# Performance work log

Hardware: AMD Instinct MI355X
Metric: run time of the kernel (lower is better)

Reference implementation:

```python
import jax, jax.numpy as jnp
import numpy as np

N, H, E, ATTR = 50000, 256, 800000, 107


def _ln(x, g, b, eps=1e-5):
    mu = jnp.mean(x, axis=-1, keepdims=True)
    v = jnp.mean((x - mu) ** 2, axis=-1, keepdims=True)
    return (x - mu) * jax.lax.rsqrt(v + eps) * g + b


def _gcn(x, src, dst, ew, W, b, n):
    # PyG GCNConv with edge_weight: add self-loops (weight 1), symmetric norm
    loop = jnp.arange(n)
    src = jnp.concatenate([src, loop])
    dst = jnp.concatenate([dst, loop])
    ew = jnp.concatenate([ew, jnp.ones((n,), ew.dtype)])
    deg = jax.ops.segment_sum(ew, dst, num_segments=n)  # [n]
    dinv = jnp.where(deg > 0, jax.lax.rsqrt(deg), 0.0)
    norm = dinv[src] * ew * dinv[dst]  # [E+n]
    h = x @ W.T  # [n,H] linear transform first
    agg = jax.ops.segment_sum(norm[:, None] * h[src], dst, num_segments=n)
    return agg + b


def setup_inputs() -> dict:
    key = jax.random.key(0)
    ks = jax.random.split(key, 12)
    s = 1.0 / np.sqrt(H)
    return {
        "x_struct": jax.random.normal(ks[0], (N, H), jnp.float32),
        "edge_index_bold": jax.random.randint(ks[1], (2, E), 0, N),
        "edge_attr_bold": jax.random.uniform(ks[2], (E,), jnp.float32),  # positive weights
        "edge_index_temp": jax.random.randint(ks[3], (2, E), 0, N),
        "edge_attr_temp": jax.random.uniform(ks[4], (E, ATTR), jnp.float32),
        "Wb": jax.random.normal(ks[5], (H, H), jnp.float32) * s,
        "bb": jnp.zeros((H,), jnp.float32),
        "Wt": jax.random.normal(ks[6], (H, H), jnp.float32) * s,
        "bt": jnp.zeros((H,), jnp.float32),
        "W1": jax.random.normal(ks[7], (H, ATTR), jnp.float32) * (1.0 / np.sqrt(ATTR)),
        "b1": jnp.zeros((H,), jnp.float32),
        "g1": jnp.ones((H,), jnp.float32),
        "be1": jnp.zeros((H,), jnp.float32),
        "W2": jax.random.normal(ks[8], (1, H), jnp.float32) * 0.01,
        "b2": jnp.ones((1,), jnp.float32),  # keep temporal edge weights positive
        "gs": jnp.ones((H,), jnp.float32),
        "bs": jnp.zeros((H,), jnp.float32),
        "gt": jnp.ones((H,), jnp.float32),
        "btn": jnp.zeros((H,), jnp.float32),
    }


def reference(x_struct, edge_attr_bold, edge_attr_temp, Wb, bb, Wt, bt,
              W1, b1, g1, be1, W2, b2, gs, bs, gt, btn,
              edge_index_bold, edge_index_temp):
    x = x_struct
    orig = x
    # BOLD-correlation GCN stage: gcn -> residual -> LN -> ReLU
    out = _gcn(x, edge_index_bold[0], edge_index_bold[1], edge_attr_bold, Wb, bb, N)
    x = jax.nn.relu(_ln(out + x, gs, bs))
    # temporal edge-weight MLP: Linear(107->H) -> LN -> ReLU -> Linear(H->1) -> squeeze
    h = jax.nn.relu(_ln(edge_attr_temp @ W1.T + b1, g1, be1))
    w = (h @ W2.T + b2)[:, 0]  # [E]
    # temporal GCN stage: gcn -> residual -> LN -> ReLU
    out = _gcn(x, edge_index_temp[0], edge_index_temp[1], w, Wt, bt, N)
    x = jax.nn.relu(_ln(out + x, gt, btn))
    # final residual with original input through struct_norm
    return _ln(x + orig, gs, bs)
```

## Files before the change

### kernel.cpp

```cpp
#include <hip/hip_runtime.h>

#define HDIM 256
#define KA 107
#define KAP 128

typedef short bf16x8 __attribute__((ext_vector_type(8)));
typedef float f32x4 __attribute__((ext_vector_type(4)));
typedef unsigned short ushort_t;

__device__ inline unsigned short f2bf(float f) {
    union { float f; unsigned u; } v; v.f = f;
    unsigned r = v.u + 0x7fff + ((v.u >> 16) & 1);
    return (unsigned short)(r >> 16);
}

__device__ inline unsigned cvt_pk_bf16(float a, float b) {
    unsigned r;
    asm("v_cvt_pk_bf16_f32 %0, %1, %2" : "=v"(r) : "v"(a), "v"(b));
    return r;
}

__device__ inline float bf_lo(unsigned u) { union { unsigned v; float f; } x; x.v = u << 16; return x.f; }
__device__ inline float bf_hi(unsigned u) { union { unsigned v; float f; } x; x.v = u & 0xffff0000u; return x.f; }

__device__ inline float4 guarded_load4(const float* p, size_t off, size_t tot) {
    if (off + 4 <= tot) return *(const float4*)(p + off);
    float4 r = {0.f, 0.f, 0.f, 0.f};
    float* rr = (float*)&r;
    for (int e = 0; e < 4; ++e) if (off + e < tot) rr[e] = p[off + e];
    return r;
}


__global__ void init_deg_kernel(float* deg, int n) {
    int i = blockIdx.x * 256 + threadIdx.x;
    if (i < n) deg[i] = 1.0f;
}

__global__ void hist_kernel(const int* __restrict__ dst, const float* __restrict__ w,
                            float* deg, int* cnt, int ne) {
    int e = blockIdx.x * 256 + threadIdx.x;
    if (e < ne) {
        int d = dst[e];
        atomicAdd(&deg[d], w[e]);
        atomicAdd(&cnt[d], 1);
    }
}

__global__ void rsqrt_kernel(float* deg, int n) {
    int i = blockIdx.x * 256 + threadIdx.x;
    if (i < n) { float d = deg[i]; deg[i] = d > 0.f ? rsqrtf(d) : 0.f; }
}

__global__ void f32_to_bf16_kernel(const float* __restrict__ in, ushort_t* __restrict__ out, int n4) {
    int i = blockIdx.x * 256 + threadIdx.x;
    if (i < n4) {
        float4 v = ((const float4*)in)[i];
        uint2 o;
        o.x = cvt_pk_bf16(v.x, v.y);
        o.y = cvt_pk_bf16(v.z, v.w);
        ((uint2*)out)[i] = o;
    }
}

__global__ __launch_bounds__(1024) void scan_kernel(const int* __restrict__ cnt,
                                                    int* __restrict__ rptr,
                                                    int* __restrict__ cur, int n) {
    const int per = (n + 1023) / 1024;
    const int tid = threadIdx.x;
    const int start = tid * per;
    const int end = min(start + per, n);
    int local = 0;
    for (int i = start; i < end; ++i) local += cnt[i];
    const int lane = tid & 63, wid = tid >> 6;
    int incl = local;
    for (int d = 1; d < 64; d <<= 1) { int m = __shfl_up(incl, d); if (lane >= d) incl += m; }
    __shared__ int wsum[16];
    if (lane == 63) wsum[wid] = incl;
    __syncthreads();
    if (tid < 16) {
        int v = wsum[tid];
        int iv = v;
        for (int d = 1; d < 16; d <<= 1) { int m = __shfl_up(iv, d, 16); if (tid >= d) iv += m; }
        wsum[tid] = iv - v;
    }
    __syncthreads();
    int run = (incl - local) + wsum[wid];
    for (int i = start; i < end; ++i) { int cc = cnt[i]; rptr[i] = run; cur[i] = run; run += cc; }
    if (start < n && end == n) rptr[n] = run;
}

__global__ void fill_kernel(const int* __restrict__ src, const int* __restrict__ dst,
                            const float* __restrict__ w, const float* __restrict__ dinv,
                            int* cur, int* __restrict__ ssrc, float* __restrict__ snrm, int ne) {
    int e = blockIdx.x * 256 + threadIdx.x;
    if (e < ne) {
        int s = src[e], d = dst[e];
        int pos = atomicAdd(&cur[d], 1);
        ssrc[pos] = s;
        snrm[pos] = dinv[s] * w[e] * dinv[d];
    }
}

__global__ __launch_bounds__(256) void agg_kernel(const ushort_t* __restrict__ Xb,
                                                  const int* __restrict__ rptr,
                                                  const int* __restrict__ ssrc,
                                                  const float* __restrict__ snrm,
                                                  const float* __restrict__ dinv,
                                                  ushort_t* __restrict__ out, int n) {
    const int v = blockIdx.x * 4 + (threadIdx.x >> 6);
    if (v >= n) return;
    const int lane = threadIdx.x & 63;
    const float dv = dinv[v];
    const uint2 xv = *(const uint2*)(Xb + (size_t)v * HDIM + lane * 4);
    const float dv2 = dv * dv;
    float a[4][4];
#pragma unroll
    for (int c = 0; c < 4; ++c)
#pragma unroll
        for (int k = 0; k < 4; ++k) a[c][k] = 0.f;
    a[0][0] = dv2 * bf_lo(xv.x); a[0][1] = dv2 * bf_hi(xv.x);
    a[0][2] = dv2 * bf_lo(xv.y); a[0][3] = dv2 * bf_hi(xv.y);

    const int b = rptr[v];
    const int total = rptr[v + 1] - b;
    uint2 pv[4]; float pn[4];
#pragma unroll
    for (int c = 0; c < 4; ++c) {
        if (c < total) {
            int s = ssrc[b + c]; pn[c] = snrm[b + c];
            pv[c] = *(const uint2*)(Xb + (size_t)s * HDIM + lane * 4);
        }
    }
    for (int base = 0; base < total; base += 4) {
#pragma unroll
        for (int c = 0; c < 4; ++c) {
            if (base + c < total) {
                uint2 cv = pv[c]; float cn = pn[c];
                int nx = base + 4 + c;
                if (nx < total) {
                    int s = ssrc[b + nx]; pn[c] = snrm[b + nx];
                    pv[c] = *(const uint2*)(Xb + (size_t)s * HDIM + lane * 4);
                }
                a[c][0] = fmaf(cn, bf_lo(cv.x), a[c][0]);
                a[c][1] = fmaf(cn, bf_hi(cv.x), a[c][1]);
                a[c][2] = fmaf(cn, bf_lo(cv.y), a[c][2]);
                a[c][3] = fmaf(cn, bf_hi(cv.y), a[c][3]);
            }
        }
    }
    float r0 = (a[0][0] + a[1][0]) + (a[2][0] + a[3][0]);
    float r1 = (a[0][1] + a[1][1]) + (a[2][1] + a[3][1]);
    float r2 = (a[0][2] + a[1][2]) + (a[2][2] + a[3][2]);
    float r3 = (a[0][3] + a[1][3]) + (a[2][3] + a[3][3]);
    uint2 o;
    o.x = cvt_pk_bf16(r0, r1);
    o.y = cvt_pk_bf16(r2, r3);
    *(uint2*)(out + (size_t)v * HDIM + lane * 4) = o;
}

__global__ void prep_w_kernel(const float* __restrict__ W, ushort_t* __restrict__ Wp,
                              int K, int KP) {
    int i = blockIdx.x * 256 + threadIdx.x;
    if (i < 256 * KP) {
        int n = i / KP, k = i - n * KP;
        Wp[i] = (k < K) ? f2bf(W[n * K + k]) : (ushort_t)0;
    }
}

__global__ __launch_bounds__(256) void mlp_mfma_kernel(
    const float* __restrict__ A,
    const ushort_t* __restrict__ Wp,
    const float* __restrict__ b1v, const float* __restrict__ g1v,
    const float* __restrict__ be1v, const float* __restrict__ W2,
    const float* __restrict__ b2s, float* __restrict__ out,
    int M, int ntiles) {
    __shared__ ushort_t As[2][64][136];
    __shared__ float ps1[64][4], ps2[64][4], pd[64][4];
    const int tid = threadIdx.x;
    const int l = tid & 63, wv = tid >> 6, g = l >> 4, c = l & 15;
    const float b2sc = b2s[0];
    const size_t totElems = (size_t)M * KA;

    for (int z = tid; z < 2 * 64 * 16; z += 256) {
        int buf = z >> 10;
        int rem = z & 1023;
        As[buf][rem >> 4][112 + (rem & 15)] = 0;
    }

    bf16x8 wreg[4][4];
    {
        const ushort_t* wb = Wp + (size_t)(wv * 64 + c) * KAP + g * 8;
#pragma unroll
        for (int ks = 0; ks < 4; ++ks)
#pragma unroll
            for (int nt = 0; nt < 4; ++nt)
                wreg[ks][nt] = *(const bf16x8*)(wb + nt * 16 * KAP + ks * 32);
    }

    const int srow = tid >> 2, sj = tid & 3;
    float4 sreg[7];

    const int t0 = blockIdx.x;
    if (t0 < ntiles) {
        const size_t roff = (size_t)(t0 * 64 + srow) * KA + sj * 4;
#pragma unroll
        for (int i = 0; i < 7; ++i) sreg[i] = guarded_load4(A, roff + i * 16, totElems);
#pragma unroll
        for (int i = 0; i < 7; ++i) {
            uint2 o;
            o.x = cvt_pk_bf16(sreg[i].x, sreg[i].y);
            o.y = cvt_pk_bf16(sreg[i].z, sreg[i].w);
            *(uint2*)&As[0][srow][sj * 4 + i * 16] = o;
        }
    }
    __syncthreads();

    int cur = 0;
    for (int t = t0; t < ntiles; t += gridDim.x) {
        const int tn = t + gridDim.x;
        const bool have_next = tn < ntiles;
        if (have_next) {
            const size_t roff = (size_t)(tn * 64 + srow) * KA + sj * 4;
#pragma unroll
            for (int i = 0; i < 7; ++i) sreg[i] = guarded_load4(A, roff + i * 16, totElems);
        }

        f32x4 acc[4][4];
#pragma unroll
        for (int rt = 0; rt < 4; ++rt)
#pragma unroll
            for (int nt = 0; nt < 4; ++nt) acc[rt][nt] = (f32x4){0.f, 0.f, 0.f, 0.f};
        __builtin_amdgcn_s_setprio(1);
#pragma unroll
        for (int ks = 0; ks < 4; ++ks) {
            bf16x8 af[4];
#pragma unroll
            for (int rt = 0; rt < 4; ++rt)
                af[rt] = *(const bf16x8*)&As[cur][rt * 16 + c][ks * 32 + g * 8];
#pragma unroll
            for (int nt = 0; nt < 4; ++nt)
#pragma unroll
                for (int rt = 0; rt < 4; ++rt)
                    acc[rt][nt] = __builtin_amdgcn_mfma_f32_16x16x32_bf16(wreg[ks][nt], af[rt], acc[rt][nt], 0, 0, 0);
        }
        __builtin_amdgcn_s_setprio(0);

        const int nb = wv * 64 + (g << 2);
        const int m0 = t * 64;
#pragma unroll
        for (int rt = 0; rt < 4; ++rt) {
            float s1 = 0.f, s2 = 0.f;
#pragma unroll
            for (int nt = 0; nt < 4; ++nt) {
                const float4 b4 = *(const float4*)(b1v + nb + nt * 16);
                f32x4 v = acc[rt][nt];
                v[0] += b4.x; v[1] += b4.y; v[2] += b4.z; v[3] += b4.w;
                acc[rt][nt] = v;
                s1 += v[0] + v[1] + v[2] + v[3];
                s2 += v[0] * v[0] + v[1] * v[1] + v[2] * v[2] + v[3] * v[3];
            }
            s1 += __shfl_xor(s1, 16); s1 += __shfl_xor(s1, 32);
            s2 += __shfl_xor(s2, 16); s2 += __shfl_xor(s2, 32);
            if (l < 16) { ps1[rt * 16 + c][wv] = s1; ps2[rt * 16 + c][wv] = s2; }
        }
        __syncthreads();
#pragma unroll
        for (int rt = 0; rt < 4; ++rt) {
            float4 p1 = *(const float4*)ps1[rt * 16 + c];
            float4 p2 = *(const float4*)ps2[rt * 16 + c];
            float s1 = p1.x + p1.y + p1.z + p1.w;
            float s2 = p2.x + p2.y + p2.z + p2.w;
            float mu = s1 * (1.f / HDIM);
            float var = s2 * (1.f / HDIM) - mu * mu;
            float rs = rsqrtf(var + 1e-5f);
            float dacc = 0.f;
#pragma unroll
            for (int nt = 0; nt < 4; ++nt) {
                const float4 g4 = *(const float4*)(g1v + nb + nt * 16);
                const float4 e4 = *(const float4*)(be1v + nb + nt * 16);
                const float4 w4 = *(const float4*)(W2 + nb + nt * 16);
                f32x4 v = acc[rt][nt];
                float y0 = fmaxf((v[0] - mu) * rs * g4.x + e4.x, 0.f);
                float y1 = fmaxf((v[1] - mu) * rs * g4.y + e4.y, 0.f);
                float y2 = fmaxf((v[2] - mu) * rs * g4.z + e4.z, 0.f);
                float y3 = fmaxf((v[3] - mu) * rs * g4.w + e4.w, 0.f);
                dacc = fmaf(y0, w4.x, dacc); dacc = fmaf(y1, w4.y, dacc);
                dacc = fmaf(y2, w4.z, dacc); dacc = fmaf(y3, w4.w, dacc);
            }
            dacc += __shfl_xor(dacc, 16); dacc += __shfl_xor(dacc, 32);
            if (l < 16) pd[rt * 16 + c][wv] = dacc;
        }
        if (have_next) {
#pragma unroll
            for (int i = 0; i < 7; ++i) {
                uint2 o;
                o.x = cvt_pk_bf16(sreg[i].x, sreg[i].y);
                o.y = cvt_pk_bf16(sreg[i].z, sreg[i].w);
                *(uint2*)&As[cur ^ 1][srow][sj * 4 + i * 16] = o;
            }
        }
        __syncthreads();
        if (tid < 64) {
            float4 p = *(const float4*)pd[tid];
            int gr = m0 + tid;
            if (gr < M) out[gr] = p.x + p.y + p.z + p.w + b2sc;
        }
        cur ^= 1;
    }
}

template <int MODE>
__global__ __launch_bounds__(256) void gemm_node_kernel(
    const ushort_t* __restrict__ A,
    const ushort_t* __restrict__ Wp,
    const float* __restrict__ bias, const float* __restrict__ res,
    const float* __restrict__ orig,
    const float* __restrict__ g1v, const float* __restrict__ b1v,
    const float* __restrict__ g2v, const float* __restrict__ b2v,
    float* __restrict__ out, ushort_t* __restrict__ out_bf, int M) {
    __shared__ ushort_t As[64][264];
    __shared__ float ps1[64][4], ps2[64][4], ps3[64][4], ps4[64][4];
    const int tid = threadIdx.x;
    const int m0 = blockIdx.x * 64;
    const int l = tid & 63, wv = tid >> 6, g = l >> 4, c = l & 15;

    {
        const int r = tid >> 2, j = tid & 3;
        const ushort_t* gsrc = A + (size_t)(m0 + r) * HDIM;
        const bool ok = (m0 + r) < M;
#pragma unroll
        for (int i = 0; i < 8; ++i) {
            const int ci = i * 4 + j;
            bf16x8 v = (bf16x8){0,0,0,0,0,0,0,0};
            if (ok) v = *(const bf16x8*)(gsrc + ci * 8);
            *(bf16x8*)&As[r][ci * 8] = v;
        }
    }
    __syncthreads();

    f32x4 acc[4][4];
#pragma unroll
    for (int rt = 0; rt < 4; ++rt)
#pragma unroll
        for (int nt = 0; nt < 4; ++nt) acc[rt][nt] = (f32x4){0.f, 0.f, 0.f, 0.f};

    const ushort_t* wb = Wp + (size_t)(wv * 64 + c) * HDIM + g * 8;
    __builtin_amdgcn_s_setprio(1);
#pragma unroll
    for (int ks = 0; ks < 8; ++ks) {
        bf16x8 af[4];
#pragma unroll
        for (int rt = 0; rt < 4; ++rt)
            af[rt] = *(const bf16x8*)&As[rt * 16 + c][ks * 32 + g * 8];
#pragma unroll
        for (int nt = 0; nt < 4; ++nt) {
            bf16x8 bfr = *(const bf16x8*)(wb + nt * 16 * HDIM + ks * 32);
#pragma unroll
            for (int rt = 0; rt < 4; ++rt)
                acc[rt][nt] = __builtin_amdgcn_mfma_f32_16x16x32_bf16(bfr, af[rt], acc[rt][nt], 0, 0, 0);
        }
    }
    __builtin_amdgcn_s_setprio(0);

    const int nb = wv * 64 + (g << 2);
#pragma unroll
    for (int rt = 0; rt < 4; ++rt) {
        const int m = m0 + rt * 16 + c;
        const bool vm = m < M;
        const float* rrow = res + (size_t)m * HDIM + nb;
        float s1 = 0.f, s2 = 0.f;
#pragma unroll
        for (int nt = 0; nt < 4; ++nt) {
            const float4 b4 = *(const float4*)(bias + nb + nt * 16);
            float4 r4 = {0.f, 0.f, 0.f, 0.f};
            if (vm) r4 = *(const float4*)(rrow + nt * 16);
            f32x4 v = acc[rt][nt];
            v[0] += b4.x + r4.x; v[1] += b4.y + r4.y;
            v[2] += b4.z + r4.z; v[3] += b4.w + r4.w;
            acc[rt][nt] = v;
            s1 += v[0] + v[1] + v[2] + v[3];
            s2 += v[0] * v[0] + v[1] * v[1] + v[2] * v[2] + v[3] * v[3];
        }
        s1 += __shfl_xor(s1, 16); s1 += __shfl_xor(s1, 32);
        s2 += __shfl_xor(s2, 16); s2 += __shfl_xor(s2, 32);
        if (l < 16) { ps1[rt * 16 + c][wv] = s1; ps2[rt * 16 + c][wv] = s2; }
    }
    __syncthreads();
#pragma unroll
    for (int rt = 0; rt < 4; ++rt) {
        const int m = m0 + rt * 16 + c;
        const bool vm = m < M;
        float4 p1 = *(const float4*)ps1[rt * 16 + c];
        float4 p2 = *(const float4*)ps2[rt * 16 + c];
        float s1 = p1.x + p1.y + p1.z + p1.w;
        float s2 = p2.x + p2.y + p2.z + p2.w;
        float mu = s1 * (1.f / HDIM);
        float var = s2 * (1.f / HDIM) - mu * mu;
        float rs = rsqrtf(var + 1e-5f);
        if constexpr (MODE == 0) {
            float* orow = out + (size_t)m * HDIM + nb;
            ushort_t* obrow = out_bf + (size_t)m * HDIM + nb;
#pragma unroll
            for (int nt = 0; nt < 4; ++nt) {
                const float4 g4 = *(const float4*)(g1v + nb + nt * 16);
                const float4 e4 = *(const float4*)(b1v + nb + nt * 16);
                f32x4 v = acc[rt][nt];
                float4 o;
                o.x = fmaxf((v[0] - mu) * rs * g4.x + e4.x, 0.f);
                o.y = fmaxf((v[1] - mu) * rs * g4.y + e4.y, 0.f);
                o.z = fmaxf((v[2] - mu) * rs * g4.z + e4.z, 0.f);
                o.w = fmaxf((v[3] - mu) * rs * g4.w + e4.w, 0.f);
                if (vm) {
                    *(float4*)(orow + nt * 16) = o;
                    uint2 ob;
                    ob.x = cvt_pk_bf16(o.x, o.y);
                    ob.y = cvt_pk_bf16(o.z, o.w);
                    *(uint2*)(obrow + nt * 16) = ob;
                }
            }
        } else {
            const float* grow = orig + (size_t)m * HDIM + nb;
            float t1 = 0.f, t2 = 0.f;
#pragma unroll
            for (int nt = 0; nt < 4; ++nt) {
                const float4 g4 = *(const float4*)(g1v + nb + nt * 16);
                const float4 e4 = *(const float4*)(b1v + nb + nt * 16);
                float4 o4 = {0.f, 0.f, 0.f, 0.f};
                if (vm) o4 = *(const float4*)(grow + nt * 16);
                f32x4 v = acc[rt][nt];
                f32x4 u;
                u[0] = fmaxf((v[0] - mu) * rs * g4.x + e4.x, 0.f) + o4.x;
                u[1] = fmaxf((v[1] - mu) * rs * g4.y + e4.y, 0.f) + o4.y;
                u[2] = fmaxf((v[2] - mu) * rs * g4.z + e4.z, 0.f) + o4.z;
                u[3] = fmaxf((v[3] - mu) * rs * g4.w + e4.w, 0.f) + o4.w;
                acc[rt][nt] = u;
                t1 += u[0] + u[1] + u[2] + u[3];
                t2 += u[0] * u[0] + u[1] * u[1] + u[2] * u[2] + u[3] * u[3];
            }
            t1 += __shfl_xor(t1, 16); t1 += __shfl_xor(t1, 32);
            t2 += __shfl_xor(t2, 16); t2 += __shfl_xor(t2, 32);
            if (l < 16) { ps3[rt * 16 + c][wv] = t1; ps4[rt * 16 + c][wv] = t2; }
        }
    }
    if constexpr (MODE == 1) {
        __syncthreads();
#pragma unroll
        for (int rt = 0; rt < 4; ++rt) {
            const int m = m0 + rt * 16 + c;
            const bool vm = m < M;
            float4 p1 = *(const float4*)ps3[rt * 16 + c];
            float4 p2 = *(const float4*)ps4[rt * 16 + c];
            float s1 = p1.x + p1.y + p1.z + p1.w;
            float s2 = p2.x + p2.y + p2.z + p2.w;
            float mu2 = s1 * (1.f / HDIM);
            float var2 = s2 * (1.f / HDIM) - mu2 * mu2;
            float rs2 = rsqrtf(var2 + 1e-5f);
            float* orow = out + (size_t)m * HDIM + nb;
#pragma unroll
            for (int nt = 0; nt < 4; ++nt) {
                const float4 g4 = *(const float4*)(g2v + nb + nt * 16);
                const float4 e4 = *(const float4*)(b2v + nb + nt * 16);
                f32x4 u = acc[rt][nt];
                float4 o;
                o.x = (u[0] - mu2) * rs2 * g4.x + e4.x;
                o.y = (u[1] - mu2) * rs2 * g4.y + e4.y;
                o.z = (u[2] - mu2) * rs2 * g4.z + e4.z;
                o.w = (u[3] - mu2) * rs2 * g4.w + e4.w;
                if (vm) *(float4*)(orow + nt * 16) = o;
            }
        }
    }
}


extern "C" void kernel_launch(void* const* d_in, const int* in_sizes, int n_in,
                              void* d_out, int out_size, void* d_ws, size_t ws_size,
                              hipStream_t stream) {
    const float* x    = (const float*)d_in[0];
    const int*   eib  = (const int*)d_in[1];
    const float* eab  = (const float*)d_in[2];
    const int*   eit  = (const int*)d_in[3];
    const float* eat  = (const float*)d_in[4];
    const float* Wb   = (const float*)d_in[5];
    const float* bb   = (const float*)d_in[6];
    const float* Wt   = (const float*)d_in[7];
    const float* bt   = (const float*)d_in[8];
    const float* W1   = (const float*)d_in[9];
    const float* b1   = (const float*)d_in[10];
    const float* g1   = (const float*)d_in[11];
    const float* be1  = (const float*)d_in[12];
    const float* W2   = (const float*)d_in[13];
    const float* b2   = (const float*)d_in[14];
    const float* gs   = (const float*)d_in[15];
    const float* bs   = (const float*)d_in[16];
    const float* gt   = (const float*)d_in[17];
    const float* btn  = (const float*)d_in[18];

    const int Nn = in_sizes[0] / HDIM;
    const int Ne = in_sizes[2];

    const int* src_b = eib;  const int* dst_b = eib + Ne;
    const int* src_t = eit;  const int* dst_t = eit + Ne;

    char* w = (char*)d_ws;
    float*    x1   = (float*)w;    w += (size_t)Nn * HDIM * 4;
    ushort_t* aggb = (ushort_t*)w; w += (size_t)Nn * HDIM * 2;
    ushort_t* xb   = (ushort_t*)w; w += (size_t)Nn * HDIM * 2;
    ushort_t* x1b  = (ushort_t*)w; w += (size_t)Nn * HDIM * 2;
    float*    wtmp = (float*)w;    w += (size_t)Ne * 4;
    float*    dinv = (float*)w;    w += (size_t)Nn * 4;
    int*      cnt  = (int*)w;      w += (size_t)Nn * 4;
    int*      rptr = (int*)w;      w += (size_t)(Nn + 4) * 4;
    int*      cur  = (int*)w;      w += (size_t)Nn * 4;
    int*      ssrc = (int*)w;      w += (size_t)Ne * 4;
    float*    snrm = (float*)w;    w += (size_t)Ne * 4;
    ushort_t* W1p  = (ushort_t*)w; w += (size_t)256 * KAP * 2;
    ushort_t* Wbp  = (ushort_t*)w; w += (size_t)256 * 256 * 2;
    ushort_t* Wtp  = (ushort_t*)w; w += (size_t)256 * 256 * 2;

    float* out = (float*)d_out;
    dim3 b256(256);
    dim3 gN((Nn + 255) / 256), gE((Ne + 255) / 256);
    dim3 gAgg((Nn + 3) / 4);
    dim3 gGemmN((Nn + 63) / 64);
    const int ntiles = (Ne + 63) / 64;
    dim3 gMlp(512);
    const int n4 = Nn * HDIM / 4;
    dim3 gCvt((n4 + 255) / 256);

    prep_w_kernel<<<dim3((256 * KAP + 255) / 256), b256, 0, stream>>>(W1, W1p, KA, KAP);
    prep_w_kernel<<<dim3((256 * 256 + 255) / 256), b256, 0, stream>>>(Wb, Wbp, 256, 256);
    prep_w_kernel<<<dim3((256 * 256 + 255) / 256), b256, 0, stream>>>(Wt, Wtp, 256, 256);
    f32_to_bf16_kernel<<<gCvt, b256, 0, stream>>>(x, xb, n4);

    init_deg_kernel<<<gN, b256, 0, stream>>>(dinv, Nn);
    hipMemsetAsync(cnt, 0, (size_t)Nn * 4, stream);
    hist_kernel<<<gE, b256, 0, stream>>>(dst_b, eab, dinv, cnt, Ne);
    rsqrt_kernel<<<gN, b256, 0, stream>>>(dinv, Nn);
    scan_kernel<<<dim3(1), dim3(1024), 0, stream>>>(cnt, rptr, cur, Nn);
    fill_kernel<<<gE, b256, 0, stream>>>(src_b, dst_b, eab, dinv, cur, ssrc, snrm, Ne);
    agg_kernel<<<gAgg, b256, 0, stream>>>(xb, rptr, ssrc, snrm, dinv, aggb, Nn);
    gemm_node_kernel<0><<<gGemmN, b256, 0, stream>>>(
        aggb, Wbp, bb, x, nullptr, gs, bs, nullptr, nullptr, x1, x1b, Nn);

    mlp_mfma_kernel<<<gMlp, b256, 0, stream>>>(
        eat, W1p, b1, g1, be1, W2, b2, wtmp, Ne, ntiles);

    init_deg_kernel<<<gN, b256, 0, stream>>>(dinv, Nn);
    hipMemsetAsync(cnt, 0, (size_t)Nn * 4, stream);
    hist_kernel<<<gE, b256, 0, stream>>>(dst_t, wtmp, dinv, cnt, Ne);
    rsqrt_kernel<<<gN, b256, 0, stream>>>(dinv, Nn);
    scan_kernel<<<dim3(1), dim3(1024), 0, stream>>>(cnt, rptr, cur, Nn);
    fill_kernel<<<gE, b256, 0, stream>>>(src_t, dst_t, wtmp, dinv, cur, ssrc, snrm, Ne);
    agg_kernel<<<gAgg, b256, 0, stream>>>(x1b, rptr, ssrc, snrm, dinv, aggb, Nn);
    gemm_node_kernel<1><<<gGemmN, b256, 0, stream>>>(
        aggb, Wtp, bt, x1, x, gt, btn, gs, bs, out, nullptr, Nn);
}
```

Before: 946.0 us.

## Raise MLP occupancy, deepen aggregation prefetch, fuse degree/count init

The edge-MLP kernel stops keeping the whole W1 fragment set in registers and reloads B fragments from global/L2 inside the k-loop. It also converts the prefetched A tile to bf16 right after loading, so the staged registers are half as wide. Together with launch_bounds(256,4) and a doubled grid, this aims for higher occupancy to hide the memory-bound load of the 800k×107 attribute matrix. The aggregation kernel keeps 8 neighbour rows in flight instead of 4 to raise memory-level parallelism, at the cost of more registers. The degree init and count memset are merged into one kernel to save a launch per stage.

```diff
diff --git a/kernel.cpp b/kernel.cpp
--- a/kernel.cpp
+++ b/kernel.cpp
@@ -32,9 +32,9 @@
 }
 
 
-__global__ void init_deg_kernel(float* deg, int n) {
+__global__ void init_kernel(float* deg, int* cnt, int n) {
     int i = blockIdx.x * 256 + threadIdx.x;
-    if (i < n) deg[i] = 1.0f;
+    if (i < n) { deg[i] = 1.0f; cnt[i] = 0; }
 }
 
 __global__ void hist_kernel(const int* __restrict__ dst, const float* __restrict__ w,
@@ -114,45 +114,43 @@
     const float dv = dinv[v];
     const uint2 xv = *(const uint2*)(Xb + (size_t)v * HDIM + lane * 4);
     const float dv2 = dv * dv;
-    float a[4][4];
-#pragma unroll
-    for (int c = 0; c < 4; ++c)
-#pragma unroll
-        for (int k = 0; k < 4; ++k) a[c][k] = 0.f;
-    a[0][0] = dv2 * bf_lo(xv.x); a[0][1] = dv2 * bf_hi(xv.x);
-    a[0][2] = dv2 * bf_lo(xv.y); a[0][3] = dv2 * bf_hi(xv.y);
+    float a0[8], a1[8], a2[8], a3[8];
+#pragma unroll
+    for (int c = 0; c < 8; ++c) { a0[c] = 0.f; a1[c] = 0.f; a2[c] = 0.f; a3[c] = 0.f; }
+    a0[0] = dv2 * bf_lo(xv.x); a1[0] = dv2 * bf_hi(xv.x);
+    a2[0] = dv2 * bf_lo(xv.y); a3[0] = dv2 * bf_hi(xv.y);
 
     const int b = rptr[v];
     const int total = rptr[v + 1] - b;
-    uint2 pv[4]; float pn[4];
-#pragma unroll
-    for (int c = 0; c < 4; ++c) {
+    uint2 pv[8]; float pn[8];
+#pragma unroll
+    for (int c = 0; c < 8; ++c) {
         if (c < total) {
             int s = ssrc[b + c]; pn[c] = snrm[b + c];
             pv[c] = *(const uint2*)(Xb + (size_t)s * HDIM + lane * 4);
         }
     }
-    for (int base = 0; base < total; base += 4) {
-#pragma unroll
-        for (int c = 0; c < 4; ++c) {
+    for (int base = 0; base < total; base += 8) {
+#pragma unroll
+        for (int c = 0; c < 8; ++c) {
             if (base + c < total) {
                 uint2 cv = pv[c]; float cn = pn[c];
-                int nx = base + 4 + c;
+                int nx = base + 8 + c;
                 if (nx < total) {
                     int s = ssrc[b + nx]; pn[c] = snrm[b + nx];
                     pv[c] = *(const uint2*)(Xb + (size_t)s * HDIM + lane * 4);
                 }
-                a[c][0] = fmaf(cn, bf_lo(cv.x), a[c][0]);
-                a[c][1] = fmaf(cn, bf_hi(cv.x), a[c][1]);
-                a[c][2] = fmaf(cn, bf_lo(cv.y), a[c][2]);
-                a[c][3] = fmaf(cn, bf_hi(cv.y), a[c][3]);
-            }
-        }
-    }
-    float r0 = (a[0][0] + a[1][0]) + (a[2][0] + a[3][0]);
-    float r1 = (a[0][1] + a[1][1]) + (a[2][1] + a[3][1]);
-    float r2 = (a[0][2] + a[1][2]) + (a[2][2] + a[3][2]);
-    float r3 = (a[0][3] + a[1][3]) + (a[2][3] + a[3][3]);
+                a0[c] = fmaf(cn, bf_lo(cv.x), a0[c]);
+                a1[c] = fmaf(cn, bf_hi(cv.x), a1[c]);
+                a2[c] = fmaf(cn, bf_lo(cv.y), a2[c]);
+                a3[c] = fmaf(cn, bf_hi(cv.y), a3[c]);
+            }
+        }
+    }
+    float r0 = ((a0[0] + a0[1]) + (a0[2] + a0[3])) + ((a0[4] + a0[5]) + (a0[6] + a0[7]));
+    float r1 = ((a1[0] + a1[1]) + (a1[2] + a1[3])) + ((a1[4] + a1[5]) + (a1[6] + a1[7]));
+    float r2 = ((a2[0] + a2[1]) + (a2[2] + a2[3])) + ((a2[4] + a2[5]) + (a2[6] + a2[7]));
+    float r3 = ((a3[0] + a3[1]) + (a3[2] + a3[3])) + ((a3[4] + a3[5]) + (a3[6] + a3[7]));
     uint2 o;
     o.x = cvt_pk_bf16(r0, r1);
     o.y = cvt_pk_bf16(r2, r3);
@@ -168,7 +166,7 @@
     }
 }
 
-__global__ __launch_bounds__(256) void mlp_mfma_kernel(
+__global__ __launch_bounds__(256, 4) void mlp_mfma_kernel(
     const float* __restrict__ A,
     const ushort_t* __restrict__ Wp,
     const float* __restrict__ b1v, const float* __restrict__ g1v,
@@ -188,31 +186,21 @@
         As[buf][rem >> 4][112 + (rem & 15)] = 0;
     }
 
-    bf16x8 wreg[4][4];
-    {
-        const ushort_t* wb = Wp + (size_t)(wv * 64 + c) * KAP + g * 8;
-#pragma unroll
-        for (int ks = 0; ks < 4; ++ks)
-#pragma unroll
-            for (int nt = 0; nt < 4; ++nt)
-                wreg[ks][nt] = *(const bf16x8*)(wb + nt * 16 * KAP + ks * 32);
-    }
-
     const int srow = tid >> 2, sj = tid & 3;
-    float4 sreg[7];
+    uint2 sreg[7];
 
     const int t0 = blockIdx.x;
     if (t0 < ntiles) {
         const size_t roff = (size_t)(t0 * 64 + srow) * KA + sj * 4;
 #pragma unroll
-        for (int i = 0; i < 7; ++i) sreg[i] = guarded_load4(A, roff + i * 16, totElems);
-#pragma unroll
         for (int i = 0; i < 7; ++i) {
-            uint2 o;
-            o.x = cvt_pk_bf16(sreg[i].x, sreg[i].y);
-            o.y = cvt_pk_bf16(sreg[i].z, sreg[i].w);
-            *(uint2*)&As[0][srow][sj * 4 + i * 16] = o;
-        }
+            float4 v = guarded_load4(A, roff + i * 16, totElems);
+            sreg[i].x = cvt_pk_bf16(v.x, v.y);
+            sreg[i].y = cvt_pk_bf16(v.z, v.w);
+        }
+#pragma unroll
+        for (int i = 0; i < 7; ++i)
+            *(uint2*)&As[0][srow][sj * 4 + i * 16] = sreg[i];
     }
     __syncthreads();
 
@@ -223,7 +211,11 @@
         if (have_next) {
             const size_t roff = (size_t)(tn * 64 + srow) * KA + sj * 4;
 #pragma unroll
-            for (int i = 0; i < 7; ++i) sreg[i] = guarded_load4(A, roff + i * 16, totElems);
+            for (int i = 0; i < 7; ++i) {
+                float4 v = guarded_load4(A, roff + i * 16, totElems);
+                sreg[i].x = cvt_pk_bf16(v.x, v.y);
+                sreg[i].y = cvt_pk_bf16(v.z, v.w);
+            }
         }
 
         f32x4 acc[4][4];
@@ -231,6 +223,7 @@
         for (int rt = 0; rt < 4; ++rt)
 #pragma unroll
             for (int nt = 0; nt < 4; ++nt) acc[rt][nt] = (f32x4){0.f, 0.f, 0.f, 0.f};
+        const ushort_t* wb = Wp + (size_t)(wv * 64 + c) * KAP + g * 8;
         __builtin_amdgcn_s_setprio(1);
 #pragma unroll
         for (int ks = 0; ks < 4; ++ks) {
@@ -239,10 +232,12 @@
             for (int rt = 0; rt < 4; ++rt)
                 af[rt] = *(const bf16x8*)&As[cur][rt * 16 + c][ks * 32 + g * 8];
 #pragma unroll
-            for (int nt = 0; nt < 4; ++nt)
+            for (int nt = 0; nt < 4; ++nt) {
+                bf16x8 bfr = *(const bf16x8*)(wb + nt * 16 * KAP + ks * 32);
 #pragma unroll
                 for (int rt = 0; rt < 4; ++rt)
-                    acc[rt][nt] = __builtin_amdgcn_mfma_f32_16x16x32_bf16(wreg[ks][nt], af[rt], acc[rt][nt], 0, 0, 0);
+                    acc[rt][nt] = __builtin_amdgcn_mfma_f32_16x16x32_bf16(bfr, af[rt], acc[rt][nt], 0, 0, 0);
+            }
         }
         __builtin_amdgcn_s_setprio(0);
 
@@ -293,12 +288,8 @@
         }
         if (have_next) {
 #pragma unroll
-            for (int i = 0; i < 7; ++i) {
-                uint2 o;
-                o.x = cvt_pk_bf16(sreg[i].x, sreg[i].y);
-                o.y = cvt_pk_bf16(sreg[i].z, sreg[i].w);
-                *(uint2*)&As[cur ^ 1][srow][sj * 4 + i * 16] = o;
-            }
+            for (int i = 0; i < 7; ++i)
+                *(uint2*)&As[cur ^ 1][srow][sj * 4 + i * 16] = sreg[i];
         }
         __syncthreads();
         if (tid < 64) {
@@ -525,7 +516,7 @@
     dim3 gAgg((Nn + 3) / 4);
     dim3 gGemmN((Nn + 63) / 64);
     const int ntiles = (Ne + 63) / 64;
-    dim3 gMlp(512);
+    dim3 gMlp(1024);
     const int n4 = Nn * HDIM / 4;
     dim3 gCvt((n4 + 255) / 256);
 
@@ -534,8 +525,7 @@
     prep_w_kernel<<<dim3((256 * 256 + 255) / 256), b256, 0, stream>>>(Wt, Wtp, 256, 256);
     f32_to_bf16_kernel<<<gCvt, b256, 0, stream>>>(x, xb, n4);
 
-    init_deg_kernel<<<gN, b256, 0, stream>>>(dinv, Nn);
-    hipMemsetAsync(cnt, 0, (size_t)Nn * 4, stream);
+    init_kernel<<<gN, b256, 0, stream>>>(dinv, cnt, Nn);
     hist_kernel<<<gE, b256, 0, stream>>>(dst_b, eab, dinv, cnt, Ne);
     rsqrt_kernel<<<gN, b256, 0, stream>>>(dinv, Nn);
     scan_kernel<<<dim3(1), dim3(1024), 0, stream>>>(cnt, rptr, cur, Nn);
@@ -547,8 +537,7 @@
     mlp_mfma_kernel<<<gMlp, b256, 0, stream>>>(
         eat, W1p, b1, g1, be1, W2, b2, wtmp, Ne, ntiles);
 
-    init_deg_kernel<<<gN, b256, 0, stream>>>(dinv, Nn);
-    hipMemsetAsync(cnt, 0, (size_t)Nn * 4, stream);
+    init_kernel<<<gN, b256, 0, stream>>>(dinv, cnt, Nn);
     hist_kernel<<<gE, b256, 0, stream>>>(dst_t, wtmp, dinv, cnt, Ne);
     rsqrt_kernel<<<gN, b256, 0, stream>>>(dinv, Nn);
     scan_kernel<<<dim3(1), dim3(1024), 0, stream>>>(cnt, rptr, cur, Nn);
```

Result: slower. 1.182 ms (+24.9%).
